# Kernel tuning notes

Measured on AMD Instinct MI355X. Metric: run time of the kernel, lower is better.

The kernel has to match this reference:

```python
import jax, jax.numpy as jnp
import numpy as np

B, N, H, OUT, L = 32, 4096, 256, 256, 4
EPS = 1e-5


def _build_edge_index(num_nodes):
    grid = int(np.sqrt(num_nodes)) + 1
    edges = []
    for i in range(num_nodes):
        col = i % grid
        if col < grid - 1 and i + 1 < num_nodes:
            edges.append([i, i + 1]); edges.append([i + 1, i])
        if i + grid < num_nodes:
            edges.append([i, i + grid]); edges.append([i + grid, i])
    return np.asarray(edges, dtype=np.int64).T  # [2, E]


def setup_inputs() -> dict:
    key = jax.random.key(0)
    ks = jax.random.split(key, 12)
    s = 0.02
    x = (jax.random.uniform(ks[0], (B, N)) < 0.1).astype(jnp.float32)  # syndrome bits
    edge_index = jnp.asarray(_build_edge_index(N))
    return {
        "x": x,
        "edge_index": edge_index,
        "proj_w": jax.random.normal(ks[1], (1, H)) * s,
        "proj_b": jnp.zeros((H,)),
        "conv_w": jax.random.normal(ks[2], (L, H, H)) * s,
        "conv_b": jnp.zeros((L, H)),
        "ln_g": jnp.ones((L, H)),
        "ln_b": jnp.zeros((L, H)),
        "h1_w": jax.random.normal(ks[3], (H, H)) * s,
        "h1_b": jnp.zeros((H,)),
        "h2_w": jax.random.normal(ks[4], (H, OUT)) * s,
        "h2_b": jnp.zeros((OUT,)),
    }


def reference(x, edge_index, proj_w, proj_b, conv_w, conv_b, ln_g, ln_b,
              h1_w, h1_b, h2_w, h2_b):
    batch, n = x.shape
    total = batch * n
    # batched edge index: replicate per sample with node offsets
    offsets = (jnp.arange(batch, dtype=edge_index.dtype) * n)
    ei = (edge_index[:, None, :] + offsets[None, :, None]).reshape(2, -1)
    src, dst = ei[0], ei[1]

    h = x.reshape(total, 1) @ proj_w + proj_b  # [total, H]

    # GCN symmetric norm with self-loops (degree = in-degree + 1)
    deg = jnp.zeros((total,), h.dtype).at[dst].add(1.0) + 1.0
    dinv_sqrt = jax.lax.rsqrt(deg)
    enorm = (dinv_sqrt[src] * dinv_sqrt[dst])[:, None]  # [E, 1]
    self_norm = (1.0 / deg)[:, None]                    # [total, 1]

    for l in range(L):
        t = h @ conv_w[l]                                   # transform
        agg = jnp.zeros_like(t).at[dst].add(enorm * t[src])  # scatter-add
        t = agg + self_norm * t + conv_b[l]
        mu = t.mean(-1, keepdims=True)
        var = ((t - mu) ** 2).mean(-1, keepdims=True)
        t = (t - mu) * jax.lax.rsqrt(var + EPS) * ln_g[l] + ln_b[l]
        h = jax.nn.relu(t)

    pooled = h.reshape(batch, n, -1).mean(axis=1)  # global_mean_pool (equal-size graphs)
    return jax.nn.relu(pooled @ h1_w + h1_b) @ h2_w + h2_b
```

## Files before the change

kernel.cpp:

```cpp
#include <hip/hip_runtime.h>
#include <cstdint>
#include <cstddef>

#define TOTAL (32*4096)
#define H 256
#define NLAYER 4

typedef __bf16 bf16x8 __attribute__((ext_vector_type(8)));
typedef float floatx4 __attribute__((ext_vector_type(4)));

__device__ __forceinline__ float u2f(unsigned int i) {
  union { unsigned int u; float f; } p; p.u = i; return p.f;
}
__device__ __forceinline__ float bf2f_lo(unsigned int u) { return u2f(u << 16); }
__device__ __forceinline__ float bf2f_hi(unsigned int u) { return u2f(u & 0xffff0000u); }
__device__ __forceinline__ unsigned int f2bf(float f) {
  union { float f; unsigned int i; } p; p.f = f;
  unsigned int r = p.i + 0x7fffu + ((p.i >> 16) & 1u);
  return r >> 16;
}

__device__ __forceinline__ float dinv_of(int n) {
  int col = n % 65;
  int deg = 1;
  deg += (n >= 1 && col != 0) ? 1 : 0;
  deg += (col != 64 && n <= 4094) ? 1 : 0;
  deg += (n >= 65) ? 1 : 0;
  deg += (n <= 4030) ? 1 : 0;
  return rsqrtf((float)deg);
}

__device__ __forceinline__ void load8(const unsigned short* p, float* v) {
  uint4 u = *reinterpret_cast<const uint4*>(p);
  v[0] = bf2f_lo(u.x); v[1] = bf2f_hi(u.x);
  v[2] = bf2f_lo(u.y); v[3] = bf2f_hi(u.y);
  v[4] = bf2f_lo(u.z); v[5] = bf2f_hi(u.z);
  v[6] = bf2f_lo(u.w); v[7] = bf2f_hi(u.w);
}
__device__ __forceinline__ uint4 pack8(const float* v) {
  uint4 u;
  u.x = f2bf(v[0]) | (f2bf(v[1]) << 16);
  u.y = f2bf(v[2]) | (f2bf(v[3]) << 16);
  u.z = f2bf(v[4]) | (f2bf(v[5]) << 16);
  u.w = f2bf(v[6]) | (f2bf(v[7]) << 16);
  return u;
}
__device__ __forceinline__ void store8(unsigned short* p, const float* v) {
  *reinterpret_cast<uint4*>(p) = pack8(v);
}
__device__ __forceinline__ void loadf8(const float* p, float* v) {
  float4 a = *reinterpret_cast<const float4*>(p);
  float4 b = *reinterpret_cast<const float4*>(p + 4);
  v[0] = a.x; v[1] = a.y; v[2] = a.z; v[3] = a.w;
  v[4] = b.x; v[5] = b.y; v[6] = b.z; v[7] = b.w;
}

__global__ void k_transpose(const float* __restrict__ w,
                            unsigned short* __restrict__ wt) {
  int idx = blockIdx.x * 256 + threadIdx.x;
  int n = idx & 255;
  int k = (idx >> 8) & 255;
  int l = idx >> 16;
  int ngrp = n >> 4, ll = n & 15, c = k >> 5, lq = (k >> 3) & 3, j = k & 7;
  wt[(size_t)l * 65536 + (ngrp * 8 + c) * 512 + (lq * 16 + ll) * 8 + j] =
      (unsigned short)f2bf(w[idx]);
}

__global__ void k_g0(const float* __restrict__ x,
                     const float* __restrict__ pw,
                     const float* __restrict__ pb,
                     unsigned short* __restrict__ G) {
  int idx = blockIdx.x * 256 + threadIdx.x;
  int gi = idx >> 5;
  int ch = idx & 31;
  int n = gi & 4095;
  int base = gi - n;
  int col = n % 65;
  float di = dinv_of(n);
  float sx = di * x[gi];
  float sc = di;
  if (n >= 1 && col != 0)     { float dj = dinv_of(n - 1);  sx += dj * x[base + n - 1];  sc += dj; }
  if (col != 64 && n <= 4094) { float dj = dinv_of(n + 1);  sx += dj * x[base + n + 1];  sc += dj; }
  if (n >= 65)                { float dj = dinv_of(n - 65); sx += dj * x[base + n - 65]; sc += dj; }
  if (n <= 4030)              { float dj = dinv_of(n + 65); sx += dj * x[base + n + 65]; sc += dj; }
  sx *= di; sc *= di;
  float w[8], b[8], o[8];
  loadf8(pw + ch * 8, w);
  loadf8(pb + ch * 8, b);
#pragma unroll
  for (int j = 0; j < 8; j++) o[j] = sx * w[j] + sc * b[j];
  store8(G + (size_t)gi * 256 + ch * 8, o);
}

template <int AGG, int POOL>
__global__ __launch_bounds__(256, 4)
void k_gemm_ln(const unsigned short* __restrict__ Hin,
               const unsigned short* __restrict__ Bf,
               const float* __restrict__ cb,
               const float* __restrict__ lg,
               const float* __restrict__ lb,
               unsigned short* __restrict__ Hout,
               float* __restrict__ pooled) {
  __shared__ alignas(16) unsigned short As[8 * 64 * 32];
  __shared__ float part[4][64][2];
  __shared__ float musr[64][2];
  const int t = threadIdx.x;
  const int w = t >> 6, lane = t & 63;
  const int lq = lane >> 4, ll = lane & 15;
  const int tile = (blockIdx.x & 7) * (gridDim.x >> 3) + (blockIdx.x >> 3);
  const int m0 = tile * 64;
  const int wc = w * 64;
  const int ar = t >> 2;
  const int ak = (t & 3) * 8;

  {
    const int gi = m0 + ar;
    const unsigned short* r0p = Hin + (size_t)gi * 256 + ak;
    if (AGG) {
      const int nd = gi & 4095;
      const int col = nd % 65;
      const float di = dinv_of(nd);
      int j1 = gi, j2 = gi, j3 = gi, j4 = gi;
      float w1 = 0.f, w2 = 0.f, w3 = 0.f, w4 = 0.f;
      if (nd >= 1 && col != 0)     { j1 = gi - 1;  w1 = dinv_of(nd - 1); }
      if (col != 64 && nd <= 4094) { j2 = gi + 1;  w2 = dinv_of(nd + 1); }
      if (nd >= 65)                { j3 = gi - 65; w3 = dinv_of(nd - 65); }
      if (nd <= 4030)              { j4 = gi + 65; w4 = dinv_of(nd + 65); }
      const unsigned short* r1p = Hin + (size_t)j1 * 256 + ak;
      const unsigned short* r2p = Hin + (size_t)j2 * 256 + ak;
      const unsigned short* r3p = Hin + (size_t)j3 * 256 + ak;
      const unsigned short* r4p = Hin + (size_t)j4 * 256 + ak;
#pragma unroll
      for (int c = 0; c < 8; c++) {
        const int k0 = c * 32;
        float a0[8], a1[8], a2[8], a3[8], a4[8];
        load8(r0p + k0, a0);
        load8(r1p + k0, a1);
        load8(r2p + k0, a2);
        load8(r3p + k0, a3);
        load8(r4p + k0, a4);
        float o[8];
#pragma unroll
        for (int q = 0; q < 8; q++)
          o[q] = di * (di * a0[q] + w1 * a1[q] + w2 * a2[q] + w3 * a3[q] + w4 * a4[q]);
        *reinterpret_cast<uint4*>(&As[c * 2048 + ar * 32 + ak]) = pack8(o);
      }
    } else {
#pragma unroll
      for (int c = 0; c < 8; c++)
        *reinterpret_cast<uint4*>(&As[c * 2048 + ar * 32 + ak]) =
            *reinterpret_cast<const uint4*>(r0p + c * 32);
    }
  }
  __syncthreads();

  floatx4 acc[4][4] = {};
  const unsigned short* bbase = Bf + (size_t)(w * 4) * 8 * 512 + lane * 8;

#pragma unroll
  for (int c = 0; c < 8; c++) {
    bf16x8 bfr[4], af[4];
#pragma unroll
    for (int cc = 0; cc < 4; cc++)
      bfr[cc] = *reinterpret_cast<const bf16x8*>(bbase + (cc * 8 + c) * 512);
#pragma unroll
    for (int r = 0; r < 4; r++)
      af[r] = *reinterpret_cast<const bf16x8*>(&As[c * 2048 + (r * 16 + ll) * 32 + lq * 8]);
#pragma unroll
    for (int r = 0; r < 4; r++)
#pragma unroll
      for (int cc = 0; cc < 4; cc++)
        acc[r][cc] = __builtin_amdgcn_mfma_f32_16x16x32_bf16(af[r], bfr[cc], acc[r][cc], 0, 0, 0);
  }

  float cbv[4], gamv[4], betv[4];
#pragma unroll
  for (int c = 0; c < 4; c++) {
    int colc = wc + c * 16 + ll;
    cbv[c] = cb[colc]; gamv[c] = lg[colc]; betv[c] = lb[colc];
  }

#pragma unroll
  for (int r = 0; r < 4; r++) {
#pragma unroll
    for (int reg = 0; reg < 4; reg++) {
      float sv = 0.f, sq = 0.f;
#pragma unroll
      for (int c = 0; c < 4; c++) {
        float v = acc[r][c][reg] + cbv[c];
        sv += v; sq += v * v;
      }
#pragma unroll
      for (int m = 8; m >= 1; m >>= 1) {
        sv += __shfl_xor(sv, m, 16);
        sq += __shfl_xor(sq, m, 16);
      }
      if (ll == 0) {
        int row = r * 16 + lq * 4 + reg;
        part[w][row][0] = sv;
        part[w][row][1] = sq;
      }
    }
  }
  __syncthreads();
  if (t < 64) {
    float s = part[0][t][0] + part[1][t][0] + part[2][t][0] + part[3][t][0];
    float q = part[0][t][1] + part[1][t][1] + part[2][t][1] + part[3][t][1];
    float mu = s * (1.0f / 256.0f);
    float var = fmaxf(q * (1.0f / 256.0f) - mu * mu, 0.0f);
    musr[t][0] = mu;
    musr[t][1] = rsqrtf(var + 1e-5f);
  }
  __syncthreads();

  if (POOL == 0) {
#pragma unroll
    for (int r = 0; r < 4; r++) {
#pragma unroll
      for (int reg = 0; reg < 4; reg++) {
        int row = r * 16 + lq * 4 + reg;
        float mu = musr[row][0], rs = musr[row][1];
#pragma unroll
        for (int c = 0; c < 4; c++) {
          float hv = (acc[r][c][reg] + cbv[c] - mu) * rs * gamv[c] + betv[c];
          hv = fmaxf(hv, 0.0f);
          Hout[(size_t)(m0 + row) * 256 + wc + c * 16 + ll] = (unsigned short)f2bf(hv);
        }
      }
    }
  } else {
    float csum[4] = {0.f, 0.f, 0.f, 0.f};
#pragma unroll
    for (int r = 0; r < 4; r++) {
#pragma unroll
      for (int reg = 0; reg < 4; reg++) {
        int row = r * 16 + lq * 4 + reg;
        float mu = musr[row][0], rs = musr[row][1];
#pragma unroll
        for (int c = 0; c < 4; c++) {
          float hv = (acc[r][c][reg] + cbv[c] - mu) * rs * gamv[c] + betv[c];
          csum[c] += fmaxf(hv, 0.0f);
        }
      }
    }
#pragma unroll
    for (int c = 0; c < 4; c++) {
      csum[c] += __shfl_xor(csum[c], 16, 64);
      csum[c] += __shfl_xor(csum[c], 32, 64);
    }
    if (lq == 0) {
      int b = m0 >> 12;
#pragma unroll
      for (int c = 0; c < 4; c++)
        atomicAdd(&pooled[b * 256 + wc + c * 16 + ll], csum[c] * (1.0f / 4096.0f));
    }
  }
}

__global__ void k_head(const float* __restrict__ pooled,
                       const float* __restrict__ w1,
                       const float* __restrict__ b1,
                       const float* __restrict__ w2,
                       const float* __restrict__ b2,
                       float* __restrict__ out) {
  const int b = blockIdx.x;
  const int t = threadIdx.x;
  __shared__ float row[256];
  __shared__ float y1[256];
  row[t] = pooled[b * 256 + t];
  __syncthreads();
  float s = b1[t];
  for (int k = 0; k < 256; k++) s += row[k] * w1[k * 256 + t];
  y1[t] = fmaxf(s, 0.0f);
  __syncthreads();
  float s2 = b2[t];
  for (int k = 0; k < 256; k++) s2 += y1[k] * w2[k * 256 + t];
  out[b * 256 + t] = s2;
}

extern "C" void kernel_launch(void* const* d_in, const int* in_sizes, int n_in,
                              void* d_out, int out_size, void* d_ws, size_t ws_size,
                              hipStream_t stream) {
  (void)in_sizes; (void)n_in; (void)out_size; (void)ws_size;
  const float* x      = (const float*)d_in[0];
  const float* proj_w = (const float*)d_in[2];
  const float* proj_b = (const float*)d_in[3];
  const float* conv_w = (const float*)d_in[4];
  const float* conv_b = (const float*)d_in[5];
  const float* ln_g   = (const float*)d_in[6];
  const float* ln_b   = (const float*)d_in[7];
  const float* h1_w   = (const float*)d_in[8];
  const float* h1_b   = (const float*)d_in[9];
  const float* h2_w   = (const float*)d_in[10];
  const float* h2_b   = (const float*)d_in[11];

  char* ws = (char*)d_ws;
  const size_t act_bytes = (size_t)TOTAL * H * 2;
  unsigned short* ha     = (unsigned short*)ws;
  unsigned short* hb     = (unsigned short*)(ws + act_bytes);
  unsigned short* wt     = (unsigned short*)(ws + 2 * act_bytes);
  float*          pooled = (float*)(ws + 2 * act_bytes + (size_t)NLAYER * H * H * 2);

  hipMemsetAsync(pooled, 0, 32 * H * sizeof(float), stream);
  k_transpose<<<NLAYER * H * H / 256, 256, 0, stream>>>(conv_w, wt);
  k_g0<<<(TOTAL * 32) / 256, 256, 0, stream>>>(x, proj_w, proj_b, ha);

  const int GB = TOTAL / 64;
  k_gemm_ln<0, 0><<<GB, 256, 0, stream>>>(ha, wt + 0 * (size_t)H * H,
      conv_b + 0 * H, ln_g + 0 * H, ln_b + 0 * H, hb, nullptr);
  k_gemm_ln<1, 0><<<GB, 256, 0, stream>>>(hb, wt + 1 * (size_t)H * H,
      conv_b + 1 * H, ln_g + 1 * H, ln_b + 1 * H, ha, nullptr);
  k_gemm_ln<1, 0><<<GB, 256, 0, stream>>>(ha, wt + 2 * (size_t)H * H,
      conv_b + 2 * H, ln_g + 2 * H, ln_b + 2 * H, hb, nullptr);
  k_gemm_ln<1, 1><<<GB, 256, 0, stream>>>(hb, wt + 3 * (size_t)H * H,
      conv_b + 3 * H, ln_g + 3 * H, ln_b + 3 * H, nullptr, pooled);

  k_head<<<32, 256, 0, stream>>>(pooled, h1_w, h1_b, h2_w, h2_b, (float*)d_out);
}
```

Baseline: 304.0 us.

## Fuse input projection into first GEMM and stage output stores through LDS

Removes the separate k_g0 kernel. The first-layer GEMM now computes the aggregated projected input directly from x, proj_w and proj_b, so the first layer no longer writes and then re-reads a full bf16 activation buffer. The non-pool epilogue also transposes its results through a padded shared-memory tile, so each thread writes 16-byte row-contiguous chunks to global memory instead of scattered 2-byte stores. The cost is a larger shared-memory footprint per block, an extra barrier, and strided 2-byte LDS reads during the transpose.

```diff
diff --git a/kernel.cpp b/kernel.cpp
--- a/kernel.cpp
+++ b/kernel.cpp
@@ -44,9 +44,6 @@
   u.z = f2bf(v[4]) | (f2bf(v[5]) << 16);
   u.w = f2bf(v[6]) | (f2bf(v[7]) << 16);
   return u;
-}
-__device__ __forceinline__ void store8(unsigned short* p, const float* v) {
-  *reinterpret_cast<uint4*>(p) = pack8(v);
 }
 __device__ __forceinline__ void loadf8(const float* p, float* v) {
   float4 a = *reinterpret_cast<const float4*>(p);
@@ -66,42 +63,21 @@
       (unsigned short)f2bf(w[idx]);
 }
 
-__global__ void k_g0(const float* __restrict__ x,
-                     const float* __restrict__ pw,
-                     const float* __restrict__ pb,
-                     unsigned short* __restrict__ G) {
-  int idx = blockIdx.x * 256 + threadIdx.x;
-  int gi = idx >> 5;
-  int ch = idx & 31;
-  int n = gi & 4095;
-  int base = gi - n;
-  int col = n % 65;
-  float di = dinv_of(n);
-  float sx = di * x[gi];
-  float sc = di;
-  if (n >= 1 && col != 0)     { float dj = dinv_of(n - 1);  sx += dj * x[base + n - 1];  sc += dj; }
-  if (col != 64 && n <= 4094) { float dj = dinv_of(n + 1);  sx += dj * x[base + n + 1];  sc += dj; }
-  if (n >= 65)                { float dj = dinv_of(n - 65); sx += dj * x[base + n - 65]; sc += dj; }
-  if (n <= 4030)              { float dj = dinv_of(n + 65); sx += dj * x[base + n + 65]; sc += dj; }
-  sx *= di; sc *= di;
-  float w[8], b[8], o[8];
-  loadf8(pw + ch * 8, w);
-  loadf8(pb + ch * 8, b);
-#pragma unroll
-  for (int j = 0; j < 8; j++) o[j] = sx * w[j] + sc * b[j];
-  store8(G + (size_t)gi * 256 + ch * 8, o);
-}
-
-template <int AGG, int POOL>
+template <int AGG, int POOL, int GPROJ>
 __global__ __launch_bounds__(256, 4)
 void k_gemm_ln(const unsigned short* __restrict__ Hin,
+               const float* __restrict__ x,
+               const float* __restrict__ pw,
+               const float* __restrict__ pb,
                const unsigned short* __restrict__ Bf,
                const float* __restrict__ cb,
                const float* __restrict__ lg,
                const float* __restrict__ lb,
                unsigned short* __restrict__ Hout,
                float* __restrict__ pooled) {
-  __shared__ alignas(16) unsigned short As[8 * 64 * 32];
+  __shared__ alignas(16) char smem[256 * 66 * 2];
+  unsigned short* As  = reinterpret_cast<unsigned short*>(smem);
+  unsigned short* Sst = reinterpret_cast<unsigned short*>(smem);
   __shared__ float part[4][64][2];
   __shared__ float musr[64][2];
   const int t = threadIdx.x;
@@ -115,17 +91,36 @@
 
   {
     const int gi = m0 + ar;
-    const unsigned short* r0p = Hin + (size_t)gi * 256 + ak;
-    if (AGG) {
-      const int nd = gi & 4095;
-      const int col = nd % 65;
-      const float di = dinv_of(nd);
+    const int nd = gi & 4095;
+    const int col = nd % 65;
+    const float di = dinv_of(nd);
+    if (GPROJ) {
+      const int base = gi - nd;
+      float sx = di * x[gi];
+      float sc = di;
+      if (nd >= 1 && col != 0)     { float dj = dinv_of(nd - 1);  sx += dj * x[base + nd - 1];  sc += dj; }
+      if (col != 64 && nd <= 4094) { float dj = dinv_of(nd + 1);  sx += dj * x[base + nd + 1];  sc += dj; }
+      if (nd >= 65)                { float dj = dinv_of(nd - 65); sx += dj * x[base + nd - 65]; sc += dj; }
+      if (nd <= 4030)              { float dj = dinv_of(nd + 65); sx += dj * x[base + nd + 65]; sc += dj; }
+      sx *= di; sc *= di;
+#pragma unroll
+      for (int c = 0; c < 8; c++) {
+        const int k0 = c * 32 + ak;
+        float wv[8], bv[8], o[8];
+        loadf8(pw + k0, wv);
+        loadf8(pb + k0, bv);
+#pragma unroll
+        for (int q = 0; q < 8; q++) o[q] = sx * wv[q] + sc * bv[q];
+        *reinterpret_cast<uint4*>(&As[c * 2048 + ar * 32 + ak]) = pack8(o);
+      }
+    } else if (AGG) {
       int j1 = gi, j2 = gi, j3 = gi, j4 = gi;
       float w1 = 0.f, w2 = 0.f, w3 = 0.f, w4 = 0.f;
       if (nd >= 1 && col != 0)     { j1 = gi - 1;  w1 = dinv_of(nd - 1); }
       if (col != 64 && nd <= 4094) { j2 = gi + 1;  w2 = dinv_of(nd + 1); }
       if (nd >= 65)                { j3 = gi - 65; w3 = dinv_of(nd - 65); }
       if (nd <= 4030)              { j4 = gi + 65; w4 = dinv_of(nd + 65); }
+      const unsigned short* r0p = Hin + (size_t)gi * 256 + ak;
       const unsigned short* r1p = Hin + (size_t)j1 * 256 + ak;
       const unsigned short* r2p = Hin + (size_t)j2 * 256 + ak;
       const unsigned short* r3p = Hin + (size_t)j3 * 256 + ak;
@@ -146,6 +141,7 @@
         *reinterpret_cast<uint4*>(&As[c * 2048 + ar * 32 + ak]) = pack8(o);
       }
     } else {
+      const unsigned short* r0p = Hin + (size_t)gi * 256 + ak;
 #pragma unroll
       for (int c = 0; c < 8; c++)
         *reinterpret_cast<uint4*>(&As[c * 2048 + ar * 32 + ak]) =
@@ -217,15 +213,35 @@
 #pragma unroll
     for (int r = 0; r < 4; r++) {
 #pragma unroll
-      for (int reg = 0; reg < 4; reg++) {
-        int row = r * 16 + lq * 4 + reg;
-        float mu = musr[row][0], rs = musr[row][1];
-#pragma unroll
-        for (int c = 0; c < 4; c++) {
-          float hv = (acc[r][c][reg] + cbv[c] - mu) * rs * gamv[c] + betv[c];
-          hv = fmaxf(hv, 0.0f);
-          Hout[(size_t)(m0 + row) * 256 + wc + c * 16 + ll] = (unsigned short)f2bf(hv);
+      for (int c = 0; c < 4; c++) {
+        int colc = wc + c * 16 + ll;
+        unsigned int p0, p1;
+        {
+          int row = r * 16 + lq * 4;
+          float h0 = fmaxf((acc[r][c][0] + cbv[c] - musr[row][0])     * musr[row][1]     * gamv[c] + betv[c], 0.0f);
+          float h1 = fmaxf((acc[r][c][1] + cbv[c] - musr[row + 1][0]) * musr[row + 1][1] * gamv[c] + betv[c], 0.0f);
+          float h2 = fmaxf((acc[r][c][2] + cbv[c] - musr[row + 2][0]) * musr[row + 2][1] * gamv[c] + betv[c], 0.0f);
+          float h3 = fmaxf((acc[r][c][3] + cbv[c] - musr[row + 3][0]) * musr[row + 3][1] * gamv[c] + betv[c], 0.0f);
+          p0 = f2bf(h0) | (f2bf(h1) << 16);
+          p1 = f2bf(h2) | (f2bf(h3) << 16);
         }
+        uint2 u; u.x = p0; u.y = p1;
+        *reinterpret_cast<uint2*>(&Sst[colc * 66 + r * 16 + lq * 4]) = u;
+      }
+    }
+    __syncthreads();
+    {
+      const int row = t >> 2;
+      const int cb0 = (t & 3) * 64;
+#pragma unroll
+      for (int g = 0; g < 8; g++) {
+        const int c0 = cb0 + g * 8;
+        uint4 u;
+        u.x = (unsigned int)Sst[(c0 + 0) * 66 + row] | ((unsigned int)Sst[(c0 + 1) * 66 + row] << 16);
+        u.y = (unsigned int)Sst[(c0 + 2) * 66 + row] | ((unsigned int)Sst[(c0 + 3) * 66 + row] << 16);
+        u.z = (unsigned int)Sst[(c0 + 4) * 66 + row] | ((unsigned int)Sst[(c0 + 5) * 66 + row] << 16);
+        u.w = (unsigned int)Sst[(c0 + 6) * 66 + row] | ((unsigned int)Sst[(c0 + 7) * 66 + row] << 16);
+        *reinterpret_cast<uint4*>(&Hout[(size_t)(m0 + row) * 256 + c0]) = u;
       }
     }
   } else {
@@ -303,17 +319,16 @@
 
   hipMemsetAsync(pooled, 0, 32 * H * sizeof(float), stream);
   k_transpose<<<NLAYER * H * H / 256, 256, 0, stream>>>(conv_w, wt);
-  k_g0<<<(TOTAL * 32) / 256, 256, 0, stream>>>(x, proj_w, proj_b, ha);
 
   const int GB = TOTAL / 64;
-  k_gemm_ln<0, 0><<<GB, 256, 0, stream>>>(ha, wt + 0 * (size_t)H * H,
-      conv_b + 0 * H, ln_g + 0 * H, ln_b + 0 * H, hb, nullptr);
-  k_gemm_ln<1, 0><<<GB, 256, 0, stream>>>(hb, wt + 1 * (size_t)H * H,
-      conv_b + 1 * H, ln_g + 1 * H, ln_b + 1 * H, ha, nullptr);
-  k_gemm_ln<1, 0><<<GB, 256, 0, stream>>>(ha, wt + 2 * (size_t)H * H,
-      conv_b + 2 * H, ln_g + 2 * H, ln_b + 2 * H, hb, nullptr);
-  k_gemm_ln<1, 1><<<GB, 256, 0, stream>>>(hb, wt + 3 * (size_t)H * H,
-      conv_b + 3 * H, ln_g + 3 * H, ln_b + 3 * H, nullptr, pooled);
+  k_gemm_ln<0, 0, 1><<<GB, 256, 0, stream>>>(nullptr, x, proj_w, proj_b,
+      wt + 0 * (size_t)H * H, conv_b + 0 * H, ln_g + 0 * H, ln_b + 0 * H, hb, nullptr);
+  k_gemm_ln<1, 0, 0><<<GB, 256, 0, stream>>>(hb, nullptr, nullptr, nullptr,
+      wt + 1 * (size_t)H * H, conv_b + 1 * H, ln_g + 1 * H, ln_b + 1 * H, ha, nullptr);
+  k_gemm_ln<1, 0, 0><<<GB, 256, 0, stream>>>(ha, nullptr, nullptr, nullptr,
+      wt + 2 * (size_t)H * H, conv_b + 2 * H, ln_g + 2 * H, ln_b + 2 * H, hb, nullptr);
+  k_gemm_ln<1, 1, 0><<<GB, 256, 0, stream>>>(hb, nullptr, nullptr, nullptr,
+      wt + 3 * (size_t)H * H, conv_b + 3 * H, ln_g + 3 * H, ln_b + 3 * H, nullptr, pooled);
 
   k_head<<<32, 256, 0, stream>>>(pooled, h1_w, h1_b, h2_w, h2_b, (float*)d_out);
 }
```

Result: slower. 332.4 us (+9.3%).
